# Kernel tuning notes

Hardware: AMD Instinct MI355X
Metric: run time of the kernel (lower is better)

Reference implementation:

```python
import jax, jax.numpy as jnp
import numpy as np

N_HEADS = 16

def setup_inputs() -> dict:
    key = jax.random.key(0)
    k1, k2, k3, k4 = jax.random.split(key, 4)
    B, T, C = 2, 2048, 1024
    x = jax.random.normal(k1, (B, T, C), dtype=jnp.float32)
    # torch nn.Linear weights: (out_features, in_features), applied as x @ W.T
    s = 1.0 / np.sqrt(C)
    Wq = jax.random.normal(k2, (C, C), dtype=jnp.float32) * s
    Wk = jax.random.normal(k3, (C, C), dtype=jnp.float32) * s
    Wv = jax.random.normal(k4, (C, C), dtype=jnp.float32) * s
    return {"x": x, "Wq": Wq, "Wk": Wk, "Wv": Wv}

def reference(x, Wq, Wk, Wv):
    B, T, C = x.shape
    H = N_HEADS
    d = C // H
    q = (x @ Wq.T).reshape(B, T, H, d)
    k = (x @ Wk.T).reshape(B, T, H, d)
    v = (x @ Wv.T).reshape(B, T, H, d)
    # NOTE: original scales by full C**-0.5, not per-head dim
    wei = jnp.einsum('bqhd,bkhd->bhqk', q, k) * (C ** -0.5)
    causal = jnp.tril(jnp.ones((T, T), dtype=bool))
    wei = jnp.where(causal, wei, -jnp.inf)
    wei = jax.nn.softmax(wei, axis=-1)
    out = jnp.einsum('bhqk,bkhd->bqhd', wei, v)
    return out.reshape(B, T, C)
```

## Files before the change

### kernel.cpp

```cpp
#include <hip/hip_runtime.h>
#include <math.h>

typedef __attribute__((ext_vector_type(8))) short short8;
typedef __attribute__((ext_vector_type(4))) float f32x4;
typedef __attribute__((ext_vector_type(16))) float f32x16;

#define BDIM 2
#define T_LEN 2048
#define CDIM 1024
#define NH 16
#define DHEAD 64
#define M_ROWS (BDIM * T_LEN)
#define NX (M_ROWS * CDIM)
#define NW (CDIM * CDIM)

#define QSCL 0.045084220f

__device__ inline unsigned short f2bf(float f) {
    union { float f; unsigned u; } v; v.f = f;
    unsigned r = v.u + 0x7fff + ((v.u >> 16) & 1);
    return (unsigned short)(r >> 16);
}

__device__ __forceinline__ void gload16(const unsigned short* g, unsigned short* l) {
    __builtin_amdgcn_global_load_lds(
        (const __attribute__((address_space(1))) void*)g,
        (__attribute__((address_space(3))) void*)l, 16, 0, 0);
}

__global__ __launch_bounds__(256) void conv_bf16(
    const float* __restrict__ x, const float* __restrict__ wq,
    const float* __restrict__ wk, const float* __restrict__ wv,
    unsigned short* __restrict__ dst)
{
    int id = blockIdx.x * 256 + threadIdx.x;
    const float* s;
    float scl = 1.0f;
    if (id < NX / 8) s = x + (size_t)id * 8;
    else {
        int r = id - NX / 8;
        int wsel = r >> 17;
        int off = r & 131071;
        const float* w = (wsel == 0) ? wq : (wsel == 1) ? wk : wv;
        if (wsel == 0) scl = QSCL;
        s = w + (size_t)off * 8;
    }
    float4 a = ((const float4*)s)[0];
    float4 b = ((const float4*)s)[1];
    union { unsigned short u[8]; short8 v; } o;
    o.u[0] = f2bf(a.x * scl); o.u[1] = f2bf(a.y * scl); o.u[2] = f2bf(a.z * scl); o.u[3] = f2bf(a.w * scl);
    o.u[4] = f2bf(b.x * scl); o.u[5] = f2bf(b.y * scl); o.u[6] = f2bf(b.z * scl); o.u[7] = f2bf(b.w * scl);
    *(short8*)(dst + (size_t)id * 8) = o.v;
}

__global__ __launch_bounds__(256) void qkv_gemm_f(
    const unsigned short* __restrict__ xb, const unsigned short* __restrict__ wb,
    unsigned short* __restrict__ qkv)
{
    __shared__ unsigned short sh[17408];
    unsigned short* A = sh;
    unsigned short* Bt = sh + 8192;
    const int z = blockIdx.z;
    const int m0 = blockIdx.x * 128;
    const int n0 = blockIdx.y * 128;
    const int tid = threadIdx.x;
    const int l = tid & 63, w = tid >> 6;
    const int li = l & 15, g4 = l >> 4;
    const int wr = w >> 1, wc = w & 1;

    const unsigned short* wsrc = wb + (size_t)z * NW;
    f32x4 acc[4][4] = {};

    for (int k0 = 0; k0 < CDIM; k0 += 64) {
        __syncthreads();
        #pragma unroll
        for (int s = 0; s < 4; ++s) {
            int c = w * 256 + s * 64 + l;
            int row = c >> 3, wcol = c & 7;
            int sw = wcol ^ (row & 7);
            gload16(xb + (size_t)(m0 + row) * CDIM + k0 + sw * 8, A + (w * 256 + s * 64) * 8);
            gload16(wsrc + (size_t)(n0 + row) * CDIM + k0 + sw * 8, Bt + (w * 256 + s * 64) * 8);
        }
        asm volatile("s_waitcnt vmcnt(0)" ::: "memory");
        __syncthreads();
        __builtin_amdgcn_s_setprio(1);
        #pragma unroll
        for (int ks = 0; ks < 2; ++ks) {
            short8 af[4], bf[4];
            #pragma unroll
            for (int fm = 0; fm < 4; ++fm) {
                int row = wr * 64 + fm * 16 + li;
                int lin = row * 128 + ks * 64 + g4 * 16;
                af[fm] = *(const short8*)((const char*)A + (lin ^ ((row & 7) << 4)));
            }
            #pragma unroll
            for (int fn = 0; fn < 4; ++fn) {
                int row = wc * 64 + fn * 16 + li;
                int lin = row * 128 + ks * 64 + g4 * 16;
                bf[fn] = *(const short8*)((const char*)Bt + (lin ^ ((row & 7) << 4)));
            }
            #pragma unroll
            for (int fm = 0; fm < 4; ++fm)
                #pragma unroll
                for (int fn = 0; fn < 4; ++fn)
                    acc[fm][fn] = __builtin_amdgcn_mfma_f32_16x16x32_bf16(af[fm], bf[fn], acc[fm][fn], 0, 0, 0);
        }
        __builtin_amdgcn_s_setprio(0);
    }
    __syncthreads();

    if (z != 2) {
        unsigned short* outp = qkv + (size_t)z * NX;
        #pragma unroll
        for (int fm = 0; fm < 4; ++fm)
            #pragma unroll
            for (int fn = 0; fn < 4; ++fn)
                #pragma unroll
                for (int r = 0; r < 4; ++r) {
                    int m = m0 + wr * 64 + fm * 16 + g4 * 4 + r;
                    int n = n0 + wc * 64 + fn * 16 + li;
                    int b = m >> 11, t = m & 2047;
                    int h = n >> 6, dd = n & 63;
                    outp[((size_t)(b * NH + h) << 17) + ((size_t)t << 6) + dd] = f2bf(acc[fm][fn][r]);
                }
    } else {
        unsigned short (*T)[136] = (unsigned short(*)[136])sh;
        #pragma unroll
        for (int fm = 0; fm < 4; ++fm)
            #pragma unroll
            for (int fn = 0; fn < 4; ++fn)
                #pragma unroll
                for (int r = 0; r < 4; ++r) {
                    int ml = wr * 64 + fm * 16 + g4 * 4 + r;
                    int nl = wc * 64 + fn * 16 + li;
                    T[nl][ml] = f2bf(acc[fm][fn][r]);
                }
        __syncthreads();
        int b = m0 >> 11;
        int t0 = m0 & 2047;
        unsigned short* vt = qkv + 2 * (size_t)NX;
        #pragma unroll
        for (int s = 0; s < 8; ++s) {
            int row = tid >> 1;
            int col = ((tid & 1) * 8 + s) * 8;
            int ng = n0 + row;
            int h = ng >> 6, dd = ng & 63;
            *(short8*)(vt + ((size_t)(b * NH + h) * 64 + dd) * T_LEN + t0 + col)
                = *(const short8*)&T[row][col];
        }
    }
}

__global__ __launch_bounds__(512, 2) void attn(
    const unsigned short* __restrict__ qkv, float* __restrict__ out)
{
    __shared__ __align__(16) unsigned short KV[2][2][2][8192];

    const int id = blockIdx.x;
    const int half = id >> 8;
    const int rr = id & 255;
    const int tI = rr >> 5;
    const int bx = half ? tI : (15 - tI);
    const int rb = rr & 31;
    const int bh = (rb & 7) * 4 + (rb >> 3);
    const int b = bh >> 4, h = bh & 15;
    const int q0 = bx * 128;
    const int tid = threadIdx.x;
    const int l = tid & 63, w = tid >> 6;
    const int hf = w >> 2, chunk = w & 3;
    const int q31 = l & 31, hi = l >> 5;

    const unsigned short* qp = qkv + (size_t)bh * (T_LEN * DHEAD);
    const unsigned short* kp = qkv + (size_t)NX + (size_t)bh * (T_LEN * DHEAD);
    const unsigned short* vp = qkv + 2 * (size_t)NX + (size_t)bh * (T_LEN * DHEAD);

    const int q0w = q0 + chunk * 32;
    const int qg = q0w + q31;

    short8 aq[4];
    #pragma unroll
    for (int ks = 0; ks < 4; ++ks)
        aq[ks] = *(const short8*)(qp + (size_t)qg * DHEAD + ks * 16 + hi * 8);

    float l_run = 0.f;
    f32x16 acc_oA[2] = {};
    f32x16 acc_oB[2] = {};

    const int T128 = bx + 1;
    const int hA = (T128 + 1) >> 1;
    const int base = hf ? hA : 0;
    const int lim  = hf ? T128 : hA;
    const int nIt  = hA;
    const int myNt64 = 2 * bx + (chunk >> 1) + 1;

    auto STAGE = [&](int j, int bf) {
        const int kv0 = j * 128;
        #pragma unroll
        for (int s = 0; s < 4; ++s) {
            int g = (chunk * 4 + s) * 64 + l;
            int krow = g >> 3, kc = g & 7;
            int ksw = kc ^ (krow & 7);
            gload16(kp + (size_t)(kv0 + krow) * DHEAD + ksw * 8, &KV[hf][bf][0][(chunk * 4 + s) * 512]);
            int sub = g >> 9, cs = g & 511;
            int vrow = cs >> 3, vc = cs & 7;
            int vsw = vc ^ (vrow & 7);
            gload16(vp + (size_t)vrow * T_LEN + kv0 + sub * 64 + vsw * 8, &KV[hf][bf][1][(chunk * 4 + s) * 512]);
        }
    };

    if (base < lim) STAGE(base, 0);
    asm volatile("s_waitcnt vmcnt(0)" ::: "memory");
    __syncthreads();

    for (int i = 0; i < nIt; ++i) {
        const int cur = i & 1;
        const int myJ = base + i;
        if (myJ + 1 < lim) STAGE(myJ + 1, cur ^ 1);

        if (myJ < lim && 2 * myJ < myNt64) {
            const char* Kbase = (const char*)&KV[hf][cur][0][0];
            const char* Vbase = (const char*)&KV[hf][cur][1][0];
            const int kv0 = myJ * 128;

            f32x16 sacc[4] = {};
            __builtin_amdgcn_s_setprio(1);
            #pragma unroll
            for (int ks = 0; ks < 4; ++ks) {
                #pragma unroll
                for (int nb = 0; nb < 4; ++nb) {
                    int row = 32 * (nb & 1) + q31;
                    int lin = row * 128 + ks * 32 + hi * 16;
                    short8 ak = *(const short8*)(Kbase + (nb >> 1) * 8192 + (lin ^ ((l & 7) << 4)));
                    sacc[nb] = __builtin_amdgcn_mfma_f32_32x32x16_bf16(ak, aq[ks], sacc[nb], 0, 0, 0);
                }
            }
            __builtin_amdgcn_s_setprio(0);

            const bool domask = (kv0 + 127 > q0w);
            if (domask) {
                #pragma unroll
                for (int nb = 0; nb < 4; ++nb)
                    #pragma unroll
                    for (int r = 0; r < 16; ++r) {
                        int kvg = kv0 + 32 * nb + (r & 3) + 8 * (r >> 2) + 4 * hi;
                        if (kvg > qg) sacc[nb][r] = -INFINITY;
                    }
            }
            float ps[16];
            #pragma unroll
            for (int r = 0; r < 16; ++r) {
                float p0 = exp2f(sacc[0][r]);
                float p1 = exp2f(sacc[1][r]);
                float p2 = exp2f(sacc[2][r]);
                float p3 = exp2f(sacc[3][r]);
                sacc[0][r] = p0; sacc[1][r] = p1; sacc[2][r] = p2; sacc[3][r] = p3;
                ps[r] = (p0 + p1) + (p2 + p3);
            }
            #pragma unroll
            for (int st = 8; st >= 1; st >>= 1)
                #pragma unroll
                for (int r2 = 0; r2 < 8; ++r2)
                    if (r2 < st) ps[r2] += ps[r2 + st];
            l_run += ps[0] + __shfl_xor(ps[0], 32);

            #pragma unroll
            for (int sub = 0; sub < 2; ++sub) {
                unsigned dw[16];
                #pragma unroll
                for (int u = 0; u < 16; ++u) {
                    float lo = sacc[2 * sub + (u >> 3)][(2 * u) & 15];
                    float hif = sacc[2 * sub + (u >> 3)][((2 * u) & 15) + 1];
                    asm("v_cvt_pk_bf16_f32 %0, %1, %2" : "=v"(dw[u]) : "v"(lo), "v"(hif));
                }
                f32x16* accp = sub ? acc_oB : acc_oA;
                __builtin_amdgcn_s_setprio(1);
                #pragma unroll
                for (int ks = 0; ks < 4; ++ks) {
                    unsigned a0 = dw[4 * ks],     b0 = dw[4 * ks + 2];
                    unsigned a1 = dw[4 * ks + 1], b1 = dw[4 * ks + 3];
                    asm("v_permlane32_swap_b32 %0, %1" : "+v"(a0), "+v"(b0));
                    asm("v_permlane32_swap_b32 %0, %1" : "+v"(a1), "+v"(b1));
                    union { unsigned u[4]; short8 v; } pb;
                    pb.u[0] = a0; pb.u[1] = a1; pb.u[2] = b0; pb.u[3] = b1;
                    #pragma unroll
                    for (int nb2 = 0; nb2 < 2; ++nb2) {
                        int row = 32 * nb2 + q31;
                        int lin = row * 128 + ks * 32 + hi * 16;
                        short8 av = *(const short8*)(Vbase + sub * 8192 + (lin ^ ((l & 7) << 4)));
                        accp[nb2] = __builtin_amdgcn_mfma_f32_32x32x16_bf16(av, pb.v, accp[nb2], 0, 0, 0);
                    }
                }
                __builtin_amdgcn_s_setprio(0);
            }
        }
        asm volatile("s_waitcnt vmcnt(0)" ::: "memory");
        __syncthreads();
    }

    f32x16 acc_o[2];
    #pragma unroll
    for (int nb2 = 0; nb2 < 2; ++nb2)
        #pragma unroll
        for (int r = 0; r < 16; ++r)
            acc_o[nb2][r] = acc_oA[nb2][r] + acc_oB[nb2][r];

    float* MB = (float*)&KV[0][0][0][0];
    float* slot = MB + (chunk * 64 + l) * 34;
    if (hf) {
        #pragma unroll
        for (int nb2 = 0; nb2 < 2; ++nb2)
            #pragma unroll
            for (int r = 0; r < 16; ++r) slot[nb2 * 16 + r] = acc_o[nb2][r];
        slot[32] = l_run;
    }
    __syncthreads();
    if (!hf) {
        float inv = 1.0f / (l_run + slot[32]);
        float* ob = out + ((size_t)(b * T_LEN + qg)) * CDIM + h * DHEAD;
        #pragma unroll
        for (int nb2 = 0; nb2 < 2; ++nb2)
            #pragma unroll
            for (int r = 0; r < 16; ++r) {
                int dd = 32 * nb2 + (r & 3) + 8 * (r >> 2) + 4 * hi;
                ob[dd] = (acc_o[nb2][r] + slot[nb2 * 16 + r]) * inv;
            }
    }
}

extern "C" void kernel_launch(void* const* d_in, const int* in_sizes, int n_in,
                              void* d_out, int out_size, void* d_ws, size_t ws_size,
                              hipStream_t stream) {
    const float* x  = (const float*)d_in[0];
    const float* Wq = (const float*)d_in[1];
    const float* Wk = (const float*)d_in[2];
    const float* Wv = (const float*)d_in[3];
    float* out = (float*)d_out;

    unsigned short* xb = (unsigned short*)d_out;
    unsigned short* wb = xb + NX;
    unsigned short* qkv = (unsigned short*)d_ws;

    conv_bf16<<<dim3((NX / 8 + 3 * NW / 8) / 256), dim3(256), 0, stream>>>(x, Wq, Wk, Wv, xb);
    qkv_gemm_f<<<dim3(M_ROWS / 128, CDIM / 128, 3), dim3(256), 0, stream>>>(xb, wb, qkv);
    attn<<<dim3(512), dim3(512), 0, stream>>>(qkv, out);
}
```

Baseline: 94.17 us.

## Pair complementary causal query blocks per workgroup to balance attention work

```diff
diff --git a/kernel.cpp b/kernel.cpp
--- a/kernel.cpp
+++ b/kernel.cpp
@@ -157,14 +157,10 @@
     __shared__ __align__(16) unsigned short KV[2][2][2][8192];
 
     const int id = blockIdx.x;
-    const int half = id >> 8;
-    const int rr = id & 255;
-    const int tI = rr >> 5;
-    const int bx = half ? tI : (15 - tI);
-    const int rb = rr & 31;
+    const int p  = id >> 5;
+    const int rb = id & 31;
     const int bh = (rb & 7) * 4 + (rb >> 3);
     const int b = bh >> 4, h = bh & 15;
-    const int q0 = bx * 128;
     const int tid = threadIdx.x;
     const int l = tid & 63, w = tid >> 6;
     const int hf = w >> 2, chunk = w & 3;
@@ -174,8 +170,10 @@
     const unsigned short* kp = qkv + (size_t)NX + (size_t)bh * (T_LEN * DHEAD);
     const unsigned short* vp = qkv + 2 * (size_t)NX + (size_t)bh * (T_LEN * DHEAD);
 
-    const int q0w = q0 + chunk * 32;
-    const int qg = q0w + q31;
+    const int qbA = 15 - p;
+    int qb = hf ? p : qbA;
+    int q0w = qb * 128 + chunk * 32;
+    int qg = q0w + q31;
 
     short8 aq[4];
     #pragma unroll
@@ -186,15 +184,14 @@
     f32x16 acc_oA[2] = {};
     f32x16 acc_oB[2] = {};
 
-    const int T128 = bx + 1;
-    const int hA = (T128 + 1) >> 1;
-    const int base = hf ? hA : 0;
-    const int lim  = hf ? T128 : hA;
-    const int nIt  = hA;
-    const int myNt64 = 2 * bx + (chunk >> 1) + 1;
-
-    auto STAGE = [&](int j, int bf) {
-        const int kv0 = j * 128;
+    const int nTiles = hf ? 8 : 9;
+    const int swU = hf ? (p + 1) : 16;
+
+    auto kv0of = [&](int t) { return ((hf && t > p) ? (t + 8 - p) : t) * 128; };
+
+    auto STAGE = [&](int t) {
+        const int kv0 = kv0of(t);
+        const int bf = t & 1;
         #pragma unroll
         for (int s = 0; s < 4; ++s) {
             int g = (chunk * 4 + s) * 64 + l;
@@ -208,19 +205,36 @@
         }
     };
 
-    if (base < lim) STAGE(base, 0);
+    STAGE(0);
     asm volatile("s_waitcnt vmcnt(0)" ::: "memory");
     __syncthreads();
 
-    for (int i = 0; i < nIt; ++i) {
-        const int cur = i & 1;
-        const int myJ = base + i;
-        if (myJ + 1 < lim) STAGE(myJ + 1, cur ^ 1);
-
-        if (myJ < lim && 2 * myJ < myNt64) {
-            const char* Kbase = (const char*)&KV[hf][cur][0][0];
-            const char* Vbase = (const char*)&KV[hf][cur][1][0];
-            const int kv0 = myJ * 128;
+    for (int i = 0; i < 9; ++i) {
+        if (hf && i == swU) {
+            float inv = 1.0f / l_run;
+            float* ob = out + ((size_t)(b * T_LEN + qg)) * CDIM + h * DHEAD;
+            #pragma unroll
+            for (int nb2 = 0; nb2 < 2; ++nb2)
+                #pragma unroll
+                for (int r = 0; r < 16; ++r) {
+                    int dd = 32 * nb2 + (r & 3) + 8 * (r >> 2) + 4 * hi;
+                    ob[dd] = (acc_oA[nb2][r] + acc_oB[nb2][r]) * inv;
+                }
+            l_run = 0.f;
+            #pragma unroll
+            for (int nb2 = 0; nb2 < 2; ++nb2)
+                #pragma unroll
+                for (int r = 0; r < 16; ++r) { acc_oA[nb2][r] = 0.f; acc_oB[nb2][r] = 0.f; }
+            qb = qbA; q0w = qb * 128 + chunk * 32; qg = q0w + q31;
+            #pragma unroll
+            for (int ks = 0; ks < 4; ++ks)
+                aq[ks] = *(const short8*)(qp + (size_t)qg * DHEAD + ks * 16 + hi * 8);
+        } else {
+            const int t = (hf && i > swU) ? i - 1 : i;
+            if (t + 1 < nTiles) STAGE(t + 1);
+            const char* Kbase = (const char*)&KV[hf][t & 1][0][0];
+            const char* Vbase = (const char*)&KV[hf][t & 1][1][0];
+            const int kv0 = kv0of(t);
 
             f32x16 sacc[4] = {};
             __builtin_amdgcn_s_setprio(1);
@@ -342,5 +356,5 @@
 
     conv_bf16<<<dim3((NX / 8 + 3 * NW / 8) / 256), dim3(256), 0, stream>>>(x, Wq, Wk, Wv, xb);
     qkv_gemm_f<<<dim3(M_ROWS / 128, CDIM / 128, 3), dim3(256), 0, stream>>>(xb, wb, qkv);
-    attn<<<dim3(512), dim3(512), 0, stream>>>(qkv, out);
-}
+    attn<<<dim3(256), dim3(512), 0, stream>>>(qkv, out);
+}
```

Result: faster. 85.51 us (-9.2%).
